# Kernel optimization log

Measured on AMD Instinct MI355X. Metric: run time of the kernel, lower is better.

## Reference

```python
import jax, jax.numpy as jnp
import numpy as np

EPS_STAB = 1e-9   # numerical_stabilizer default
BN_EPS = 1e-5     # flax BatchNorm default epsilon


def setup_inputs() -> dict:
    key = jax.random.key(0)
    ks = jax.random.split(key, 5)
    B, N, C = 2, 4096, 512
    s = 1.0 / np.sqrt(C)
    d = {"inputs": jax.random.normal(ks[0], (B, N, C), jnp.float32)}
    # 1x1 convs == pointwise linear maps [C_in, C_out] + bias
    for i, w in enumerate(["Wq", "Wk", "Wv", "Wo"]):
        d[w] = jax.random.normal(ks[1 + i], (C, C), jnp.float32) * s
    for b in ["bq", "bk", "bv", "bo"]:
        d[b] = jnp.zeros((C,), jnp.float32)
    # BatchNorm (inference: use_running_average=True since train=False)
    d["bn_scale"] = jnp.ones((C,), jnp.float32)
    d["bn_bias"] = jnp.zeros((C,), jnp.float32)
    d["bn_mean"] = jnp.zeros((C,), jnp.float32)
    d["bn_var"] = jnp.ones((C,), jnp.float32)
    return d


def reference(inputs, Wq, bq, Wk, bk, Wv, bv, Wo, bo,
              bn_scale, bn_bias, bn_mean, bn_var):
    # QKV via 1x1 conv == dense projection. [B, N, C]
    q = inputs @ Wq + bq
    k = inputs @ Wk + bk
    v = inputs @ Wv + bv
    # scores [B, M, N]; softmax over last axis (N)
    att = jax.nn.softmax(jnp.einsum('bmc,bnc->bmn', q, k), axis=-1)
    # non-standard renorm: divide by column sums (axis=1 == M axis)
    att = att / (EPS_STAB + jnp.sum(att, axis=1, keepdims=True))
    # faithful to einsum '...MN,...NC->...NC': sum attention over M, scale v
    out = v * jnp.sum(att, axis=1)[..., None]
    # output 1x1 conv
    out = out @ Wo + bo
    # BatchNorm with running stats (feature axis -1)
    out = (out - bn_mean) * jax.lax.rsqrt(bn_var + BN_EPS) * bn_scale + bn_bias
    return jax.nn.relu(out) + inputs
```

## Files before the change

kernel.cpp:

```cpp
#include <hip/hip_runtime.h>
#include <hip/hip_bf16.h>

typedef unsigned short u16;
typedef unsigned int u32;
typedef __attribute__((ext_vector_type(8))) short short8;
typedef __attribute__((ext_vector_type(4))) float f32x4;

__device__ __forceinline__ u16 f2bf(float f) {
    union { float f; unsigned u; } v; v.f = f;
    unsigned r = v.u + 0x7fffu + ((v.u >> 16) & 1u);
    return (u16)(r >> 16);
}
__device__ __forceinline__ float bf2f(u16 h) {
    union { unsigned u; float f; } v; v.u = ((unsigned)h) << 16;
    return v.f;
}

__device__ __forceinline__ float fexp2(float x) {
#if __has_builtin(__builtin_amdgcn_exp2f)
    return __builtin_amdgcn_exp2f(x);
#else
    return __expf(x * 0.6931471805599453f);
#endif
}

__device__ __forceinline__ void async_cp16(const u16* g, u16* l) {
    __builtin_amdgcn_global_load_lds(
        (const __attribute__((address_space(1))) void*)g,
        (__attribute__((address_space(3))) void*)l, 16, 0, 0);
}


__device__ __forceinline__ void gemm512(const u16* __restrict__ A,
                                        const u16* __restrict__ B,
                                        u16* As, u16* Bs,
                                        f32x4 acc[4][4], int tid) {
    const int lane = tid & 63, w = tid >> 6;
    const int quad = lane >> 4, l15 = lane & 15;
    const int wm = tid >> 7, wn = (tid >> 6) & 1;
    const int Gw = lane ^ ((lane >> 3) & 7);
    const int srow = Gw >> 2;
    const int scol = (Gw & 3) * 8;
    const int arow0 = w * 32 + srow, arow1 = arow0 + 16;
    u16* la0 = As + (w * 2 + 0) * 512;
    u16* la1 = As + (w * 2 + 1) * 512;
    u16* lb0 = Bs + (w * 2 + 0) * 512;
    u16* lb1 = Bs + (w * 2 + 1) * 512;
    const int Pr8 = ((l15 * 4 + quad) ^ (l15 >> 1)) * 8;
    for (int k0 = 0; k0 < 512; k0 += 32) {
        __syncthreads();
        async_cp16(A + (size_t)arow0 * 512 + k0 + scol, la0);
        async_cp16(A + (size_t)arow1 * 512 + k0 + scol, la1);
        async_cp16(B + (size_t)arow0 * 512 + k0 + scol, lb0);
        async_cp16(B + (size_t)arow1 * 512 + k0 + scol, lb1);
        __syncthreads();
        short8 af[4], bfr[4];
#pragma unroll
        for (int i = 0; i < 4; i++)
            af[i] = *(const short8*)&As[(wm * 64 + i * 16) * 32 + Pr8];
#pragma unroll
        for (int j = 0; j < 4; j++)
            bfr[j] = *(const short8*)&Bs[(wn * 64 + j * 16) * 32 + Pr8];
#pragma unroll
        for (int i = 0; i < 4; i++)
#pragma unroll
            for (int j = 0; j < 4; j++)
                acc[i][j] = __builtin_amdgcn_mfma_f32_16x16x32_bf16(
                    af[i], bfr[j], acc[i][j], 0, 0, 0);
    }
}

__device__ __forceinline__ void gemm512_r64(const u16* __restrict__ A,
                                            const u16* __restrict__ B,
                                            u16* As, u16* Bs,
                                            f32x4 acc[2][4], int tid) {
    const int lane = tid & 63, w = tid >> 6;
    const int quad = lane >> 4, l15 = lane & 15;
    const int wm = tid >> 7, wn = (tid >> 6) & 1;
    const int Gw = lane ^ ((lane >> 3) & 7);
    const int srow = Gw >> 2;
    const int scol = (Gw & 3) * 8;
    const int arowA = w * 16 + srow;
    const int arowB0 = (w * 2 + 0) * 16 + srow;
    const int arowB1 = (w * 2 + 1) * 16 + srow;
    u16* la = As + w * 512;
    u16* lb0 = Bs + (w * 2 + 0) * 512;
    u16* lb1 = Bs + (w * 2 + 1) * 512;
    const int Pr8 = ((l15 * 4 + quad) ^ (l15 >> 1)) * 8;
    for (int k0 = 0; k0 < 512; k0 += 32) {
        __syncthreads();
        async_cp16(A + (size_t)arowA * 512 + k0 + scol, la);
        async_cp16(B + (size_t)arowB0 * 512 + k0 + scol, lb0);
        async_cp16(B + (size_t)arowB1 * 512 + k0 + scol, lb1);
        __syncthreads();
        short8 af[2], bfr[4];
#pragma unroll
        for (int i = 0; i < 2; i++)
            af[i] = *(const short8*)&As[(wm * 32 + i * 16) * 32 + Pr8];
#pragma unroll
        for (int j = 0; j < 4; j++)
            bfr[j] = *(const short8*)&Bs[(wn * 64 + j * 16) * 32 + Pr8];
#pragma unroll
        for (int i = 0; i < 2; i++)
#pragma unroll
            for (int j = 0; j < 4; j++)
                acc[i][j] = __builtin_amdgcn_mfma_f32_16x16x32_bf16(
                    af[i], bfr[j], acc[i][j], 0, 0, 0);
    }
}

__global__ void prep(const float* __restrict__ X, const float* __restrict__ W0,
                     const float* __restrict__ W1, const float* __restrict__ W2,
                     const float* __restrict__ W3, u16* __restrict__ Xb,
                     u16* __restrict__ T0, u16* __restrict__ T1,
                     u16* __restrict__ T2, u16* __restrict__ T3) {
    __shared__ float tile[32][33];
    int id = blockIdx.x, tid = threadIdx.x;
    if (id < 4096) {
        int idx = (id * 256 + tid) * 4;
        float4 v = *(const float4*)&X[idx];
        ushort4 o;
        o.x = f2bf(v.x); o.y = f2bf(v.y); o.z = f2bf(v.z); o.w = f2bf(v.w);
        *(ushort4*)&Xb[idx] = o;
        return;
    }
    int t = id - 4096;
    int z = t >> 8, rem = t & 255;
    int bo_ = (rem & 15) * 32, bi = (rem >> 4) * 32;
    const float* src; u16* dst;
    switch (z) {
        case 0: src = W0; dst = T0; break;
        case 1: src = W1; dst = T1; break;
        case 2: src = W2; dst = T2; break;
        default: src = W3; dst = T3; break;
    }
    int tx = tid & 31, ty = tid >> 5;
#pragma unroll
    for (int s = 0; s < 4; s++) {
        int i = bi + ty + s * 8;
        tile[ty + s * 8][tx] = src[i * 512 + bo_ + tx];
    }
    __syncthreads();
#pragma unroll
    for (int s = 0; s < 4; s++) {
        int o = bo_ + ty + s * 8;
        dst[o * 512 + bi + tx] = f2bf(tile[tx][ty + s * 8]);
    }
}

__global__ __launch_bounds__(256) void gemm_qkv(
    const u16* __restrict__ Xb, const u16* __restrict__ Wall,
    const float* __restrict__ bq, const float* __restrict__ bk,
    const float* __restrict__ bv, u16* __restrict__ Qall) {
    __shared__ __align__(16) u16 As[128 * 32];
    __shared__ __align__(16) u16 Bs[128 * 32];
    int tid = threadIdx.x;
    int m0 = blockIdx.x * 128, n0 = blockIdx.y * 128, z = blockIdx.z;
    const u16* Bt = Wall + (size_t)z * 262144 + (size_t)n0 * 512;
    const float* bias = (z == 0) ? bq : (z == 1) ? bk : bv;
    const float qs = (z == 0) ? 1.44269504088896340736f : 1.0f;
    u16* C = Qall + (size_t)z * 4194304;
    f32x4 acc[4][4];
#pragma unroll
    for (int i = 0; i < 4; i++)
#pragma unroll
        for (int j = 0; j < 4; j++) acc[i][j] = (f32x4){0.f, 0.f, 0.f, 0.f};
    gemm512(Xb + (size_t)m0 * 512, Bt, As, Bs, acc, tid);
    int lane = tid & 63, quad = lane >> 4, l15 = lane & 15;
    int wm = tid >> 7, wn = (tid >> 6) & 1;
#pragma unroll
    for (int j = 0; j < 4; j++) {
        int n = n0 + wn * 64 + j * 16 + l15;
        float bvv = bias[n];
#pragma unroll
        for (int i = 0; i < 4; i++)
#pragma unroll
            for (int rg = 0; rg < 4; rg++) {
                int m = m0 + wm * 64 + i * 16 + quad * 4 + rg;
                C[(size_t)m * 512 + n] = f2bf((acc[i][j][rg] + bvv) * qs);
            }
    }
}

__global__ __launch_bounds__(256) void attn_pass1p(
    const u16* __restrict__ Qb, const u16* __restrict__ Kb,
    float2* __restrict__ statsP, u32* __restrict__ Pbuf, int b0) {
    __shared__ __align__(16) u16 As[128 * 32];
    __shared__ __align__(16) u16 Bs[128 * 32];
    int tid = threadIdx.x;
    int mblk = blockIdx.x, nch = blockIdx.y, zb = blockIdx.z, b = b0 + zb;
    const u16* Q = Qb + ((size_t)(b * 4096 + mblk * 128)) * 512;
    int lane = tid & 63, quad = lane >> 4, l15 = lane & 15;
    int wm = tid >> 7, wn = (tid >> 6) & 1;
    for (int nt = 0; nt < 2; nt++) {
        const u16* K = Kb + ((size_t)(b * 4096 + nch * 256 + nt * 128)) * 512;
        f32x4 acc[4][4];
#pragma unroll
        for (int i = 0; i < 4; i++)
#pragma unroll
            for (int j = 0; j < 4; j++) acc[i][j] = (f32x4){0.f, 0.f, 0.f, 0.f};
        gemm512(Q, K, As, Bs, acc, tid);
        u32* Pt = Pbuf + (((size_t)(zb * 32 + mblk) * 16 + nch) * 2 + nt) * 8192;
        int ch = nch * 4 + nt * 2 + wn;
#pragma unroll
        for (int i = 0; i < 4; i++)
#pragma unroll
            for (int rg = 0; rg < 4; rg++) {
                float v0 = acc[i][0][rg], v1 = acc[i][1][rg];
                float v2 = acc[i][2][rg], v3 = acc[i][3][rg];
                float Mt = fmaxf(fmaxf(v0, v1), fmaxf(v2, v3));
                Mt = fmaxf(Mt, __shfl_xor(Mt, 1));
                Mt = fmaxf(Mt, __shfl_xor(Mt, 2));
                Mt = fmaxf(Mt, __shfl_xor(Mt, 4));
                Mt = fmaxf(Mt, __shfl_xor(Mt, 8));
                float p0 = fexp2(v0 - Mt), p1 = fexp2(v1 - Mt);
                float p2 = fexp2(v2 - Mt), p3 = fexp2(v3 - Mt);
                float L = p0 + p1 + p2 + p3;
                L += __shfl_xor(L, 1);
                L += __shfl_xor(L, 2);
                L += __shfl_xor(L, 4);
                L += __shfl_xor(L, 8);
                Pt[((i * 4 + rg) * 2 + 0) * 256 + tid] =
                    (u32)f2bf(p0) | ((u32)f2bf(p1) << 16);
                Pt[((i * 4 + rg) * 2 + 1) * 256 + tid] =
                    (u32)f2bf(p2) | ((u32)f2bf(p3) << 16);
                if (l15 == 0)
                    statsP[((size_t)(b * 64 + ch)) * 4096 + mblk * 128 +
                           wm * 64 + i * 16 + quad * 4 + rg] =
                        make_float2(Mt, L);
            }
    }
}

__global__ void reduce_stats2(const float2* __restrict__ statsP,
                              float* __restrict__ cstat, float* __restrict__ Sg,
                              int b0) {
    int t = blockIdx.x * 256 + threadIdx.x;
    int b = b0 + (t >> 12), m = t & 4095;
    const float2* sp = statsP + (size_t)b * 64 * 4096 + m;
    float M = -INFINITY;
#pragma unroll 4
    for (int ch = 0; ch < 64; ch++) M = fmaxf(M, sp[(size_t)ch * 4096].x);
    float Z = 0.f;
#pragma unroll 4
    for (int ch = 0; ch < 64; ch++) {
        float2 p = sp[(size_t)ch * 4096];
        Z += p.y * fexp2(p.x - M);
    }
    cstat[b * 4096 + m] = M + __log2f(Z);
    Sg[b * 4096 + m] = 0.f;
}

__global__ __launch_bounds__(256) void colsum(
    const u32* __restrict__ Pbuf, const float2* __restrict__ statsP,
    const float* __restrict__ cstat, float* __restrict__ Sg, int b0) {
    int tid = threadIdx.x, lane = tid & 63;
    int wm = tid >> 7, wn = (tid >> 6) & 1, quad = lane >> 4;
    int nch = blockIdx.x, nt = blockIdx.y & 1, mgrp = blockIdx.y >> 1;
    int zb = blockIdx.z, b = b0 + zb;
    int ch = nch * 4 + nt * 2 + wn;
    const float2* Sp = statsP + ((size_t)(b * 64 + ch)) * 4096;
    const float* Cp = cstat + (size_t)b * 4096;
    float cp[4] = {0.f, 0.f, 0.f, 0.f};
    for (int mb = 0; mb < 4; mb++) {
        int mblk = mgrp * 4 + mb;
        const u32* Pt =
            Pbuf + (((size_t)(zb * 32 + mblk) * 16 + nch) * 2 + nt) * 8192;
#pragma unroll
        for (int i = 0; i < 4; i++) {
            int r0 = mblk * 128 + wm * 64 + i * 16 + quad * 4;
            float4 s01 = *(const float4*)&Sp[r0];
            float4 s23 = *(const float4*)&Sp[r0 + 2];
            float4 cv = *(const float4*)&Cp[r0];
            float fv[4] = {fexp2(s01.x - cv.x), fexp2(s01.z - cv.y),
                           fexp2(s23.x - cv.z), fexp2(s23.z - cv.w)};
#pragma unroll
            for (int rg = 0; rg < 4; rg++) {
                u32 ua = Pt[((i * 4 + rg) * 2 + 0) * 256 + tid];
                u32 ub = Pt[((i * 4 + rg) * 2 + 1) * 256 + tid];
                cp[0] += bf2f((u16)(ua & 0xffff)) * fv[rg];
                cp[1] += bf2f((u16)(ua >> 16)) * fv[rg];
                cp[2] += bf2f((u16)(ub & 0xffff)) * fv[rg];
                cp[3] += bf2f((u16)(ub >> 16)) * fv[rg];
            }
        }
    }
#pragma unroll
    for (int j = 0; j < 4; j++) {
        float s = cp[j];
        s += __shfl_xor(s, 16);
        s += __shfl_xor(s, 32);
        if (lane < 16)
            atomicAdd(&Sg[b * 4096 + nch * 256 + nt * 128 + wn * 64 + j * 16 + lane], s);
    }
}

__global__ __launch_bounds__(256) void legacy_pass1(
    const u16* __restrict__ Qb, const u16* __restrict__ Kb,
    float2* __restrict__ statsP) {
    __shared__ __align__(16) u16 As[128 * 32];
    __shared__ __align__(16) u16 Bs[128 * 32];
    int tid = threadIdx.x;
    int mblk = blockIdx.x, nch = blockIdx.y, b = blockIdx.z;
    const u16* Q = Qb + ((size_t)(b * 4096 + mblk * 128)) * 512;
    int lane = tid & 63, quad = lane >> 4, l15 = lane & 15;
    int wm = tid >> 7, wn = (tid >> 6) & 1;
    float runM[4][4], runL[4][4];
#pragma unroll
    for (int i = 0; i < 4; i++)
#pragma unroll
        for (int rg = 0; rg < 4; rg++) { runM[i][rg] = -INFINITY; runL[i][rg] = 0.f; }
    for (int nt = 0; nt < 2; nt++) {
        const u16* K = Kb + ((size_t)(b * 4096 + nch * 256 + nt * 128)) * 512;
        f32x4 acc[4][4];
#pragma unroll
        for (int i = 0; i < 4; i++)
#pragma unroll
            for (int j = 0; j < 4; j++) acc[i][j] = (f32x4){0.f, 0.f, 0.f, 0.f};
        gemm512(Q, K, As, Bs, acc, tid);
#pragma unroll
        for (int i = 0; i < 4; i++)
#pragma unroll
            for (int rg = 0; rg < 4; rg++) {
                float v0 = acc[i][0][rg], v1 = acc[i][1][rg];
                float v2 = acc[i][2][rg], v3 = acc[i][3][rg];
                float vm = fmaxf(fmaxf(v0, v1), fmaxf(v2, v3));
                float mo = runM[i][rg];
                if (vm > mo - 30.f) {
                    float nm = fmaxf(mo, vm);
                    runL[i][rg] = runL[i][rg] * fexp2(mo - nm) +
                                  fexp2(v0 - nm) + fexp2(v1 - nm) +
                                  fexp2(v2 - nm) + fexp2(v3 - nm);
                    runM[i][rg] = nm;
                }
            }
    }
#pragma unroll
    for (int i = 0; i < 4; i++)
#pragma unroll
        for (int rg = 0; rg < 4; rg++) {
            float M = runM[i][rg];
            float Mf = M;
#pragma unroll
            for (int d = 1; d < 16; d <<= 1) Mf = fmaxf(Mf, __shfl_xor(Mf, d));
            float L = runL[i][rg] * fexp2(M - Mf);
#pragma unroll
            for (int d = 1; d < 16; d <<= 1) L += __shfl_xor(L, d);
            if (l15 == 0)
                statsP[((size_t)(b * 32 + nch * 2 + wn)) * 4096 +
                       mblk * 128 + wm * 64 + i * 16 + quad * 4 + rg] =
                    make_float2(Mf, L);
        }
}

__global__ void legacy_reduce(const float2* __restrict__ statsP,
                              float* __restrict__ cstat, float* __restrict__ Sg) {
    int t = blockIdx.x * 256 + threadIdx.x;
    int b = t >> 12, m = t & 4095;
    const float2* sp = statsP + (size_t)b * 32 * 4096 + m;
    float M = -INFINITY;
#pragma unroll 4
    for (int ch = 0; ch < 32; ch++) M = fmaxf(M, sp[(size_t)ch * 4096].x);
    float L = 0.f;
#pragma unroll 4
    for (int ch = 0; ch < 32; ch++) {
        float2 p = sp[(size_t)ch * 4096];
        L += p.y * fexp2(p.x - M);
    }
    cstat[t] = M + __log2f(L);
    Sg[t] = 0.f;
}

__global__ __launch_bounds__(256) void legacy_pass2(
    const u16* __restrict__ Qb, const u16* __restrict__ Kb,
    const float* __restrict__ cstat, float* __restrict__ Sg) {
    __shared__ __align__(16) u16 As[128 * 32];
    __shared__ __align__(16) u16 Bs[128 * 32];
    int tid = threadIdx.x;
    int nblk = blockIdx.x, mch = blockIdx.y, b = blockIdx.z;
    const u16* K = Kb + ((size_t)(b * 4096 + nblk * 128)) * 512;
    int lane = tid & 63, quad = lane >> 4;
    int wm = tid >> 7, wn = (tid >> 6) & 1;
    float cp0 = 0.f, cp1 = 0.f, cp2 = 0.f, cp3 = 0.f;
    for (int mt = 0; mt < 2; mt++) {
        int m0 = mch * 256 + mt * 128;
        const u16* Q = Qb + ((size_t)(b * 4096 + m0)) * 512;
        f32x4 acc[4][4];
#pragma unroll
        for (int i = 0; i < 4; i++)
#pragma unroll
            for (int j = 0; j < 4; j++) acc[i][j] = (f32x4){0.f, 0.f, 0.f, 0.f};
        gemm512(Q, K, As, Bs, acc, tid);
        float4 c4[4];
#pragma unroll
        for (int i = 0; i < 4; i++)
            c4[i] = *(const float4*)&cstat[b * 4096 + m0 + wm * 64 + i * 16 + quad * 4];
#pragma unroll
        for (int i = 0; i < 4; i++) {
            float cc[4] = {c4[i].x, c4[i].y, c4[i].z, c4[i].w};
#pragma unroll
            for (int rg = 0; rg < 4; rg++) {
                float c = cc[rg];
                float v0 = acc[i][0][rg] - c, v1 = acc[i][1][rg] - c;
                float v2 = acc[i][2][rg] - c, v3 = acc[i][3][rg] - c;
                float vm = fmaxf(fmaxf(v0, v1), fmaxf(v2, v3));
                if (vm > -60.f) {
                    cp0 += fexp2(v0); cp1 += fexp2(v1);
                    cp2 += fexp2(v2); cp3 += fexp2(v3);
                }
            }
        }
    }
    float cps[4] = {cp0, cp1, cp2, cp3};
#pragma unroll
    for (int j = 0; j < 4; j++) {
        float s = cps[j];
        s += __shfl_xor(s, 16);
        s += __shfl_xor(s, 32);
        if (lane < 16)
            atomicAdd(&Sg[b * 4096 + nblk * 128 + wn * 64 + j * 16 + lane], s);
    }
}

__global__ __launch_bounds__(256) void gemm_final(
    const u16* __restrict__ A, const u16* __restrict__ Bt,
    const float* __restrict__ Sg, const float* __restrict__ bo,
    const float* __restrict__ g, const float* __restrict__ bb,
    const float* __restrict__ mean, const float* __restrict__ var,
    const float* __restrict__ X, float* __restrict__ out) {
    __shared__ __align__(16) u16 As[64 * 32];
    __shared__ __align__(16) u16 Bs[128 * 32];
    int tid = threadIdx.x;
    int m0 = blockIdx.x * 64, n0 = blockIdx.y * 128;
    f32x4 acc[2][4];
#pragma unroll
    for (int i = 0; i < 2; i++)
#pragma unroll
        for (int j = 0; j < 4; j++) acc[i][j] = (f32x4){0.f, 0.f, 0.f, 0.f};
    gemm512_r64(A + (size_t)m0 * 512, Bt + (size_t)n0 * 512, As, Bs, acc, tid);
    int lane = tid & 63, quad = lane >> 4, l15 = lane & 15;
    int wm = tid >> 7, wn = (tid >> 6) & 1;
    float sc[2][4];
#pragma unroll
    for (int i = 0; i < 2; i++) {
        float4 s = *(const float4*)&Sg[m0 + wm * 32 + i * 16 + quad * 4];
        float v[4] = {s.x, s.y, s.z, s.w};
#pragma unroll
        for (int rg = 0; rg < 4; rg++) sc[i][rg] = v[rg] / (1e-9f + v[rg]);
    }
#pragma unroll
    for (int j = 0; j < 4; j++) {
        int n = n0 + wn * 64 + j * 16 + l15;
        float aj = rsqrtf(var[n] + 1e-5f) * g[n];
        float cj = bb[n] - mean[n] * aj;
        float bj = bo[n];
#pragma unroll
        for (int i = 0; i < 2; i++)
#pragma unroll
            for (int rg = 0; rg < 4; rg++) {
                int m = m0 + wm * 32 + i * 16 + quad * 4 + rg;
                float x = acc[i][j][rg] * sc[i][rg] + bj;
                float y = x * aj + cj;
                out[(size_t)m * 512 + n] = fmaxf(y, 0.f) + X[(size_t)m * 512 + n];
            }
    }
}

extern "C" void kernel_launch(void* const* d_in, const int* in_sizes, int n_in,
                              void* d_out, int out_size, void* d_ws, size_t ws_size,
                              hipStream_t stream) {
    const float* X  = (const float*)d_in[0];
    const float* Wq = (const float*)d_in[1];
    const float* Wk = (const float*)d_in[2];
    const float* Wv = (const float*)d_in[3];
    const float* Wo = (const float*)d_in[4];
    const float* bq = (const float*)d_in[5];
    const float* bk = (const float*)d_in[6];
    const float* bv = (const float*)d_in[7];
    const float* bo = (const float*)d_in[8];
    const float* g    = (const float*)d_in[9];
    const float* bb   = (const float*)d_in[10];
    const float* mean = (const float*)d_in[11];
    const float* var  = (const float*)d_in[12];
    float* out = (float*)d_out;

    char* ws = (char*)d_ws;
    u16* Xb  = (u16*)(ws + 0);
    u16* Wqt = (u16*)(ws + 8388608);
    u16* Wot = (u16*)(ws + 9961472);
    u16* Qb  = (u16*)(ws + 10485760);
    u16* Kb  = (u16*)(ws + 18874368);
    u16* Vb  = (u16*)(ws + 27262976);
    float2* statsP = (float2*)(ws + 35651584);
    float* cstat   = (float*)(ws + 39845888);
    float* Sg      = (float*)(ws + 39878656);
    u32* Pbuf      = (u32*)(ws + 39911424);

    const size_t FULL_NEED  = 39911424ull + 67108864ull;
    const size_t BATCH_NEED = 39911424ull + 33554432ull;

    prep<<<5120, 256, 0, stream>>>(X, Wq, Wk, Wv, Wo, Xb, Wqt, Wqt + 262144,
                                   Wqt + 524288, Wot);
    gemm_qkv<<<dim3(64, 4, 3), 256, 0, stream>>>(Xb, Wqt, bq, bk, bv, Qb);

    if (ws_size >= FULL_NEED) {
        attn_pass1p<<<dim3(32, 16, 2), 256, 0, stream>>>(Qb, Kb, statsP, Pbuf, 0);
        reduce_stats2<<<32, 256, 0, stream>>>(statsP, cstat, Sg, 0);
        colsum<<<dim3(16, 16, 2), 256, 0, stream>>>(Pbuf, statsP, cstat, Sg, 0);
    } else if (ws_size >= BATCH_NEED) {
        for (int b = 0; b < 2; b++) {
            attn_pass1p<<<dim3(32, 16, 1), 256, 0, stream>>>(Qb, Kb, statsP, Pbuf, b);
            reduce_stats2<<<16, 256, 0, stream>>>(statsP, cstat, Sg, b);
            colsum<<<dim3(16, 16, 1), 256, 0, stream>>>(Pbuf, statsP, cstat, Sg, b);
        }
    } else {
        legacy_pass1<<<dim3(32, 16, 2), 256, 0, stream>>>(Qb, Kb, statsP);
        legacy_reduce<<<32, 256, 0, stream>>>(statsP, cstat, Sg);
        legacy_pass2<<<dim3(32, 16, 2), 256, 0, stream>>>(Qb, Kb, cstat, Sg);
    }
    gemm_final<<<dim3(128, 4), 256, 0, stream>>>(Vb, Wot, Sg, bo, g, bb, mean, var,
                                                 X, out);
}
```

Before: 222.9 us.

## Store softmax probabilities as fp8 and fuse row-stat reduction into colsum

Stores the materialized probability tiles as fp8 (e4m3, offset by 2^8 before scaling) instead of bf16, halving the size of the intermediate P buffer written and read back. The row-stat reduction kernel is folded into colsum, with each block recomputing the logsumexp for its rows into shared memory. Sg zeroing moves into an extra prep block. This removes a launch and cuts memory traffic, but adds redundant stat recomputation across blocks and lowers the precision of the attention column sums.

```diff
diff --git a/kernel.cpp b/kernel.cpp
--- a/kernel.cpp
+++ b/kernel.cpp
@@ -10,10 +10,6 @@
     union { float f; unsigned u; } v; v.f = f;
     unsigned r = v.u + 0x7fffu + ((v.u >> 16) & 1u);
     return (u16)(r >> 16);
-}
-__device__ __forceinline__ float bf2f(u16 h) {
-    union { unsigned u; float f; } v; v.u = ((unsigned)h) << 16;
-    return v.f;
 }
 
 __device__ __forceinline__ float fexp2(float x) {
@@ -23,6 +19,48 @@
     return __expf(x * 0.6931471805599453f);
 #endif
 }
+
+#if __has_builtin(__builtin_amdgcn_cvt_pk_fp8_f32) && \
+    __has_builtin(__builtin_amdgcn_cvt_f32_fp8)
+#define FP8_HW 1
+#else
+#define FP8_HW 0
+#endif
+
+#if !FP8_HW
+__device__ __forceinline__ u32 sw_fp8(float x) {
+    union { float f; u32 u; } v; v.f = x;
+    int E = (int)(v.u >> 23) - 127;
+    if (x < 0.001953125f) return 0;
+    if (E < -6) return (u32)(x * 512.0f + 0.5f);
+    u32 m = v.u & 0x7fffffu;
+    u32 r = (m + 0x80000u) >> 20;
+    u32 bits = ((u32)(E + 7) << 3) + r;
+    return bits > 0x7eu ? 0x7eu : bits;
+}
+__device__ __forceinline__ float sw_fp8d(u32 b) {
+    u32 e = (b >> 3) & 15u, m = b & 7u;
+    if (e == 0) return (float)m * 0.001953125f;
+    union { u32 u; float f; } v; v.u = ((e + 120u) << 23) | (m << 20);
+    return v.f;
+}
+#endif
+
+__device__ __forceinline__ u32 fp8x4_pack(float p0, float p1, float p2, float p3) {
+#if FP8_HW
+    u32 v = (u32)__builtin_amdgcn_cvt_pk_fp8_f32(p0, p1, 0, false);
+    v = (u32)__builtin_amdgcn_cvt_pk_fp8_f32(p2, p3, (int)v, true);
+    return v;
+#else
+    return sw_fp8(p0) | (sw_fp8(p1) << 8) | (sw_fp8(p2) << 16) | (sw_fp8(p3) << 24);
+#endif
+}
+
+#if FP8_HW
+#define FP8_DEC(v, s) __builtin_amdgcn_cvt_f32_fp8((int)(v), (s))
+#else
+#define FP8_DEC(v, s) sw_fp8d(((v) >> ((s) * 8)) & 0xffu)
+#endif
 
 __device__ __forceinline__ void async_cp16(const u16* g, u16* l) {
     __builtin_amdgcn_global_load_lds(
@@ -113,9 +151,16 @@
                      const float* __restrict__ W1, const float* __restrict__ W2,
                      const float* __restrict__ W3, u16* __restrict__ Xb,
                      u16* __restrict__ T0, u16* __restrict__ T1,
-                     u16* __restrict__ T2, u16* __restrict__ T3) {
+                     u16* __restrict__ T2, u16* __restrict__ T3,
+                     float* __restrict__ Sg) {
     __shared__ float tile[32][33];
     int id = blockIdx.x, tid = threadIdx.x;
+    if (id == 5120) {
+        float4 z = {0.f, 0.f, 0.f, 0.f};
+#pragma unroll
+        for (int t = 0; t < 8; t++) ((float4*)Sg)[tid + t * 256] = z;
+        return;
+    }
     if (id < 4096) {
         int idx = (id * 256 + tid) * 4;
         float4 v = *(const float4*)&X[idx];
@@ -184,11 +229,11 @@
 
 __global__ __launch_bounds__(256) void attn_pass1p(
     const u16* __restrict__ Qb, const u16* __restrict__ Kb,
-    float2* __restrict__ statsP, u32* __restrict__ Pbuf, int b0) {
+    float2* __restrict__ statsP, u32* __restrict__ Pbuf) {
     __shared__ __align__(16) u16 As[128 * 32];
     __shared__ __align__(16) u16 Bs[128 * 32];
     int tid = threadIdx.x;
-    int mblk = blockIdx.x, nch = blockIdx.y, zb = blockIdx.z, b = b0 + zb;
+    int mblk = blockIdx.x, nch = blockIdx.y, b = blockIdx.z;
     const u16* Q = Qb + ((size_t)(b * 4096 + mblk * 128)) * 512;
     int lane = tid & 63, quad = lane >> 4, l15 = lane & 15;
     int wm = tid >> 7, wn = (tid >> 6) & 1;
@@ -200,7 +245,7 @@
 #pragma unroll
             for (int j = 0; j < 4; j++) acc[i][j] = (f32x4){0.f, 0.f, 0.f, 0.f};
         gemm512(Q, K, As, Bs, acc, tid);
-        u32* Pt = Pbuf + (((size_t)(zb * 32 + mblk) * 16 + nch) * 2 + nt) * 8192;
+        u32* Pt = Pbuf + (((size_t)(b * 32 + mblk) * 16 + nch) * 2 + nt) * 4096;
         int ch = nch * 4 + nt * 2 + wn;
 #pragma unroll
         for (int i = 0; i < 4; i++)
@@ -213,75 +258,71 @@
                 Mt = fmaxf(Mt, __shfl_xor(Mt, 2));
                 Mt = fmaxf(Mt, __shfl_xor(Mt, 4));
                 Mt = fmaxf(Mt, __shfl_xor(Mt, 8));
-                float p0 = fexp2(v0 - Mt), p1 = fexp2(v1 - Mt);
-                float p2 = fexp2(v2 - Mt), p3 = fexp2(v3 - Mt);
+                float e8 = Mt - 8.0f;
+                float p0 = fexp2(v0 - e8), p1 = fexp2(v1 - e8);
+                float p2 = fexp2(v2 - e8), p3 = fexp2(v3 - e8);
+                Pt[(i * 4 + rg) * 256 + tid] = fp8x4_pack(p0, p1, p2, p3);
                 float L = p0 + p1 + p2 + p3;
                 L += __shfl_xor(L, 1);
                 L += __shfl_xor(L, 2);
                 L += __shfl_xor(L, 4);
                 L += __shfl_xor(L, 8);
-                Pt[((i * 4 + rg) * 2 + 0) * 256 + tid] =
-                    (u32)f2bf(p0) | ((u32)f2bf(p1) << 16);
-                Pt[((i * 4 + rg) * 2 + 1) * 256 + tid] =
-                    (u32)f2bf(p2) | ((u32)f2bf(p3) << 16);
                 if (l15 == 0)
                     statsP[((size_t)(b * 64 + ch)) * 4096 + mblk * 128 +
                            wm * 64 + i * 16 + quad * 4 + rg] =
-                        make_float2(Mt, L);
+                        make_float2(Mt, L * 0.00390625f);
             }
     }
 }
 
-__global__ void reduce_stats2(const float2* __restrict__ statsP,
-                              float* __restrict__ cstat, float* __restrict__ Sg,
-                              int b0) {
-    int t = blockIdx.x * 256 + threadIdx.x;
-    int b = b0 + (t >> 12), m = t & 4095;
-    const float2* sp = statsP + (size_t)b * 64 * 4096 + m;
-    float M = -INFINITY;
-#pragma unroll 4
-    for (int ch = 0; ch < 64; ch++) M = fmaxf(M, sp[(size_t)ch * 4096].x);
-    float Z = 0.f;
-#pragma unroll 4
-    for (int ch = 0; ch < 64; ch++) {
-        float2 p = sp[(size_t)ch * 4096];
-        Z += p.y * fexp2(p.x - M);
-    }
-    cstat[b * 4096 + m] = M + __log2f(Z);
-    Sg[b * 4096 + m] = 0.f;
-}
-
-__global__ __launch_bounds__(256) void colsum(
+__global__ __launch_bounds__(256) void colsum_fused(
     const u32* __restrict__ Pbuf, const float2* __restrict__ statsP,
-    const float* __restrict__ cstat, float* __restrict__ Sg, int b0) {
+    float* __restrict__ Sg) {
+    __shared__ float cbuf[512];
     int tid = threadIdx.x, lane = tid & 63;
     int wm = tid >> 7, wn = (tid >> 6) & 1, quad = lane >> 4;
     int nch = blockIdx.x, nt = blockIdx.y & 1, mgrp = blockIdx.y >> 1;
-    int zb = blockIdx.z, b = b0 + zb;
+    int b = blockIdx.z;
     int ch = nch * 4 + nt * 2 + wn;
+#pragma unroll
+    for (int h = 0; h < 2; h++) {
+        int row = mgrp * 512 + h * 256 + tid;
+        const float2* sp = statsP + (size_t)b * 64 * 4096 + row;
+        float M = -INFINITY;
+#pragma unroll 4
+        for (int c2 = 0; c2 < 64; c2++) M = fmaxf(M, sp[(size_t)c2 * 4096].x);
+        float Z = 0.f;
+#pragma unroll 4
+        for (int c2 = 0; c2 < 64; c2++) {
+            float2 p = sp[(size_t)c2 * 4096];
+            Z += p.y * fexp2(p.x - M);
+        }
+        cbuf[h * 256 + tid] = M + __log2f(Z);
+    }
+    __syncthreads();
     const float2* Sp = statsP + ((size_t)(b * 64 + ch)) * 4096;
-    const float* Cp = cstat + (size_t)b * 4096;
     float cp[4] = {0.f, 0.f, 0.f, 0.f};
     for (int mb = 0; mb < 4; mb++) {
         int mblk = mgrp * 4 + mb;
         const u32* Pt =
-            Pbuf + (((size_t)(zb * 32 + mblk) * 16 + nch) * 2 + nt) * 8192;
+            Pbuf + (((size_t)(b * 32 + mblk) * 16 + nch) * 2 + nt) * 4096;
 #pragma unroll
         for (int i = 0; i < 4; i++) {
             int r0 = mblk * 128 + wm * 64 + i * 16 + quad * 4;
             float4 s01 = *(const float4*)&Sp[r0];
             float4 s23 = *(const float4*)&Sp[r0 + 2];
-            float4 cv = *(const float4*)&Cp[r0];
-            float fv[4] = {fexp2(s01.x - cv.x), fexp2(s01.z - cv.y),
-                           fexp2(s23.x - cv.z), fexp2(s23.z - cv.w)};
+            float4 cv = *(const float4*)&cbuf[r0 - mgrp * 512];
+            float fv[4] = {fexp2(s01.x - 8.0f - cv.x),
+                           fexp2(s01.z - 8.0f - cv.y),
+                           fexp2(s23.x - 8.0f - cv.z),
+                           fexp2(s23.z - 8.0f - cv.w)};
 #pragma unroll
             for (int rg = 0; rg < 4; rg++) {
-                u32 ua = Pt[((i * 4 + rg) * 2 + 0) * 256 + tid];
-                u32 ub = Pt[((i * 4 + rg) * 2 + 1) * 256 + tid];
-                cp[0] += bf2f((u16)(ua & 0xffff)) * fv[rg];
-                cp[1] += bf2f((u16)(ua >> 16)) * fv[rg];
-                cp[2] += bf2f((u16)(ub & 0xffff)) * fv[rg];
-                cp[3] += bf2f((u16)(ub >> 16)) * fv[rg];
+                u32 e = Pt[(i * 4 + rg) * 256 + tid];
+                cp[0] += FP8_DEC(e, 0) * fv[rg];
+                cp[1] += FP8_DEC(e, 1) * fv[rg];
+                cp[2] += FP8_DEC(e, 2) * fv[rg];
+                cp[3] += FP8_DEC(e, 3) * fv[rg];
             }
         }
     }
@@ -492,27 +533,19 @@
     u16* Kb  = (u16*)(ws + 18874368);
     u16* Vb  = (u16*)(ws + 27262976);
     float2* statsP = (float2*)(ws + 35651584);
-    float* cstat   = (float*)(ws + 39845888);
-    float* Sg      = (float*)(ws + 39878656);
+    float* Sg      = (float*)(ws + 39845888);
+    float* cstat   = (float*)(ws + 39878656);
     u32* Pbuf      = (u32*)(ws + 39911424);
 
-    const size_t FULL_NEED  = 39911424ull + 67108864ull;
-    const size_t BATCH_NEED = 39911424ull + 33554432ull;
-
-    prep<<<5120, 256, 0, stream>>>(X, Wq, Wk, Wv, Wo, Xb, Wqt, Wqt + 262144,
-                                   Wqt + 524288, Wot);
+    const size_t FULL_NEED = 39911424ull + 33554432ull;
+
+    prep<<<5121, 256, 0, stream>>>(X, Wq, Wk, Wv, Wo, Xb, Wqt, Wqt + 262144,
+                                   Wqt + 524288, Wot, Sg);
     gemm_qkv<<<dim3(64, 4, 3), 256, 0, stream>>>(Xb, Wqt, bq, bk, bv, Qb);
 
     if (ws_size >= FULL_NEED) {
-        attn_pass1p<<<dim3(32, 16, 2), 256, 0, stream>>>(Qb, Kb, statsP, Pbuf, 0);
-        reduce_stats2<<<32, 256, 0, stream>>>(statsP, cstat, Sg, 0);
-        colsum<<<dim3(16, 16, 2), 256, 0, stream>>>(Pbuf, statsP, cstat, Sg, 0);
-    } else if (ws_size >= BATCH_NEED) {
-        for (int b = 0; b < 2; b++) {
-            attn_pass1p<<<dim3(32, 16, 1), 256, 0, stream>>>(Qb, Kb, statsP, Pbuf, b);
-            reduce_stats2<<<16, 256, 0, stream>>>(statsP, cstat, Sg, b);
-            colsum<<<dim3(16, 16, 1), 256, 0, stream>>>(Pbuf, statsP, cstat, Sg, b);
-        }
+        attn_pass1p<<<dim3(32, 16, 2), 256, 0, stream>>>(Qb, Kb, statsP, Pbuf);
+        colsum_fused<<<dim3(16, 16, 2), 256, 0, stream>>>(Pbuf, statsP, Sg);
     } else {
         legacy_pass1<<<dim3(32, 16, 2), 256, 0, stream>>>(Qb, Kb, statsP);
         legacy_reduce<<<32, 256, 0, stream>>>(statsP, cstat, Sg);
```

Result: slower. 232.5 us (+4.3%).
